# Kernel optimization log

Hardware: AMD Instinct MI355X
Metric: run time of the kernel (lower is better)

Reference implementation:

```python
import jax, jax.numpy as jnp
import numpy as np

INV_SMOOTHNESS = 0.1  # matches __init__ default


def setup_inputs() -> dict:
    key = jax.random.key(0)
    B, N, W, H = 128, 64, 64, 64
    # polygon vertices in pixel coordinates [0, W) x [0, H)
    vertices = jax.random.uniform(key, (B, N, 2), dtype=jnp.float32) * jnp.array([W, H], jnp.float32)
    return {"vertices": vertices, "width": W, "height": H}


def reference(vertices, width, height):
    """Soft polygon rasterization (mode='mask').

    For every pixel p: d2 = min over edges of squared point-to-segment distance;
    sign = +1 if p inside polygon (even-odd rule) else -1;
    out = sigmoid(sign * d2 / inv_smoothness).
    Matches the native CUDA forward_rasterize for MODE_MASK.
    """
    B, N, _ = vertices.shape
    dt = vertices.dtype
    xs = jnp.arange(width, dtype=dt)
    ys = jnp.arange(height, dtype=dt)
    px, py = jnp.meshgrid(xs, ys, indexing="xy")         # [H, W]
    p = jnp.stack([px.ravel(), py.ravel()], axis=-1)       # [P, 2], P = H*W

    a = vertices                                           # [B, N, 2] edge start
    b = jnp.roll(vertices, -1, axis=1)                     # [B, N, 2] edge end
    d = b - a                                              # [B, N, 2]
    dd = jnp.maximum(jnp.sum(d * d, axis=-1), 1e-12)       # [B, N]

    # point-to-segment squared distance, vectorized over pixels and edges
    pa = p[None, :, None, :] - a[:, None, :, :]            # [B, P, N, 2]
    t = jnp.clip(jnp.einsum("bpnc,bnc->bpn", pa, d) / dd[:, None, :], 0.0, 1.0)
    diff = pa - t[..., None] * d[:, None, :, :]            # [B, P, N, 2]
    dist2 = jnp.sum(diff * diff, axis=-1)                  # [B, P, N]
    min_d2 = jnp.min(dist2, axis=-1)                       # [B, P]

    # even-odd (pnpoly) inside test
    x = p[:, 0][None, :, None]                             # [1, P, 1]
    y = p[:, 1][None, :, None]
    ax, ay = a[:, None, :, 0], a[:, None, :, 1]            # [B, 1, N]
    bx, by = b[:, None, :, 0], b[:, None, :, 1]
    cond = (ay > y) != (by > y)                            # edge straddles scanline
    denom = jnp.where(cond, by - ay, 1.0)
    x_int = (bx - ax) * (y - ay) / denom + ax              # edge x at scanline y
    crossings = jnp.sum((cond & (x < x_int)).astype(jnp.int32), axis=-1)  # [B, P]
    sign = jnp.where((crossings % 2) == 1, 1.0, -1.0).astype(dt)

    out = jax.nn.sigmoid(sign * min_d2 / INV_SMOOTHNESS)
    return out.reshape(B, height, width)
```

## Files before the change

kernel.cpp:

```cpp
#include <hip/hip_runtime.h>


#define EDGE(E0, E1, DA, DB)                                       \
    {                                                              \
        float pay  = py - E0.y;                                    \
        float pdyr = pay * E1.y;                                   \
        float xint = fmaf(pay, E1.z, E0.x);                        \
        bool  cond = (E0.y > py) != (E1.w > py);                   \
        float paxa = px0 - E0.x;                                   \
        float paxb = paxa + 1.0f;                                  \
        float ta = fminf(fmaxf(fmaf(paxa, E1.x, pdyr), 0.0f), 1.0f); \
        float tb = fminf(fmaxf(fmaf(paxb, E1.x, pdyr), 0.0f), 1.0f); \
        float exa = fmaf(-ta, E0.z, paxa);                         \
        float eya = fmaf(-ta, E0.w, pay);                          \
        float exb = fmaf(-tb, E0.z, paxb);                         \
        float eyb = fmaf(-tb, E0.w, pay);                          \
        DA = fmaf(exa, exa, eya * eya);                            \
        DB = fmaf(exb, exb, eyb * eyb);                            \
        pm0 ^= __ballot(cond && (px0 < xint));                     \
        pm1 ^= __ballot(cond && (px1 < xint));                     \
    }

__global__ __launch_bounds__(256, 4) void softpoly_kernel(
    const float* __restrict__ verts, float* __restrict__ out)
{
    __shared__ float4 e0[64];
    __shared__ float4 e1[64];

    const int tid = threadIdx.x;
    const int b   = blockIdx.x >> 3;

    if (tid < 64) {
        const float2* vp = (const float2*)(verts + (b << 7));
        float2 a = vp[tid];
        float2 c = vp[(tid + 1) & 63];
        float dx = c.x - a.x, dy = c.y - a.y;
        float dd = fmaxf(fmaf(dx, dx, dy * dy), 1e-12f);
        float rdd = 1.0f / dd;
        e0[tid] = make_float4(a.x, a.y, dx, dy);
        e1[tid] = make_float4(dx * rdd, dy * rdd, dx / dy, c.y);
    }
    __syncthreads();

    const int row = ((blockIdx.x & 7) << 3) + (tid >> 5);
    const float py  = (float)row;
    const float px0 = (float)((tid & 31) << 1);
    const float px1 = px0 + 1.0f;

    float md0 = 1e30f, md1 = 1e30f;
    unsigned long long pm0 = 0ull, pm1 = 0ull;

    #pragma unroll 2
    for (int n = 0; n < 64; n += 2) {
        const float4 A0 = e0[n],     A1 = e1[n];
        const float4 B0 = e0[n + 1], B1 = e1[n + 1];
        float dA0, dA1, dB0, dB1;
        EDGE(A0, A1, dA0, dA1)
        EDGE(B0, B1, dB0, dB1)
        md0 = fminf(md0, fminf(dA0, dB0));
        md1 = fminf(md1, fminf(dA1, dB1));
    }

    const int lane = tid & 63;
    const float s0 = ((pm0 >> lane) & 1ull) ? 10.0f : -10.0f;
    const float s1 = ((pm1 >> lane) & 1ull) ? 10.0f : -10.0f;
    float2 r;
    r.x = 1.0f / (1.0f + __expf(-s0 * md0));
    r.y = 1.0f / (1.0f + __expf(-s1 * md1));
    ((float2*)out)[(((b << 6) + row) << 5) + (tid & 31)] = r;
}

extern "C" void kernel_launch(void* const* d_in, const int* in_sizes, int n_in,
                              void* d_out, int out_size, void* d_ws, size_t ws_size,
                              hipStream_t stream) {
    const float* verts = (const float*)d_in[0];
    float* out = (float*)d_out;
    const int B = out_size >> 12;
    softpoly_kernel<<<dim3(B * 8), dim3(256), 0, stream>>>(verts, out);
}
```

Baseline: 16.06 us.

## Use packed FP32 math and four pixels per thread in soft polygon kernel

Each thread now covers four adjacent pixels instead of two, and the grid shrinks to four blocks per batch. The per-edge distance math uses inline-asm v_pk_fma/v_pk_mul/v_pk_add to handle two pixels per instruction. The aim is to amortize edge loads and per-edge scalar setup over more pixels and to halve the VALU instruction count for the distance computation. The trade-offs are higher register pressure, the removal of the occupancy hint from launch_bounds, and fewer blocks in flight.

After: 19.04 us. +18.5%, slower.

```diff
diff --git a/kernel.cpp b/kernel.cpp
--- a/kernel.cpp
+++ b/kernel.cpp
@@ -1,34 +1,57 @@
 #include <hip/hip_runtime.h>
 
 
-#define EDGE(E0, E1, DA, DB)                                       \
-    {                                                              \
-        float pay  = py - E0.y;                                    \
-        float pdyr = pay * E1.y;                                   \
-        float xint = fmaf(pay, E1.z, E0.x);                        \
-        bool  cond = (E0.y > py) != (E1.w > py);                   \
-        float paxa = px0 - E0.x;                                   \
-        float paxb = paxa + 1.0f;                                  \
-        float ta = fminf(fmaxf(fmaf(paxa, E1.x, pdyr), 0.0f), 1.0f); \
-        float tb = fminf(fmaxf(fmaf(paxb, E1.x, pdyr), 0.0f), 1.0f); \
-        float exa = fmaf(-ta, E0.z, paxa);                         \
-        float eya = fmaf(-ta, E0.w, pay);                          \
-        float exb = fmaf(-tb, E0.z, paxb);                         \
-        float eyb = fmaf(-tb, E0.w, pay);                          \
-        DA = fmaf(exa, exa, eya * eya);                            \
-        DB = fmaf(exb, exb, eyb * eyb);                            \
-        pm0 ^= __ballot(cond && (px0 < xint));                     \
-        pm1 ^= __ballot(cond && (px1 < xint));                     \
+typedef float f32x2 __attribute__((ext_vector_type(2)));
+typedef float f32x4 __attribute__((ext_vector_type(4)));
+
+#define PK_FMA(d,a,b,c)      asm("v_pk_fma_f32 %0, %1, %2, %3" : "=v"(d) : "v"(a), "v"(b), "v"(c))
+#define PK_MUL(d,a,b)        asm("v_pk_mul_f32 %0, %1, %2" : "=v"(d) : "v"(a), "v"(b))
+#define PK_FMA_BLO(d,a,B,c)  asm("v_pk_fma_f32 %0, %1, %2, %3 op_sel_hi:[1,0,1]" : "=v"(d) : "v"(a), "v"(B), "v"(c))
+#define PK_NFMA_BLO(d,a,B,c) asm("v_pk_fma_f32 %0, %1, %2, %3 op_sel_hi:[1,0,1] neg_lo:[1,0,0] neg_hi:[1,0,0]" : "=v"(d) : "v"(a), "v"(B), "v"(c))
+#define PK_NFMA_BHI(d,a,B,c) asm("v_pk_fma_f32 %0, %1, %2, %3 op_sel:[0,1,0] op_sel_hi:[1,1,1] neg_lo:[1,0,0] neg_hi:[1,0,0]" : "=v"(d) : "v"(a), "v"(B), "v"(c))
+#define PK_SUB_BLO(d,a,B)    asm("v_pk_add_f32 %0, %1, %2 op_sel_hi:[1,0] neg_lo:[0,1] neg_hi:[0,1]" : "=v"(d) : "v"(a), "v"(B))
+#define PK_SUB_BHI(d,a,B)    asm("v_pk_add_f32 %0, %1, %2 op_sel:[0,1] op_sel_hi:[1,1] neg_lo:[0,1] neg_hi:[0,1]" : "=v"(d) : "v"(a), "v"(B))
+#define PK_MUL_BHI(d,a,B)    asm("v_pk_mul_f32 %0, %1, %2 op_sel:[0,1] op_sel_hi:[1,1]" : "=v"(d) : "v"(a), "v"(B))
+
+#define EDGE(E0, E1, DA, DB)                                        \
+    {                                                               \
+        f32x2 E0lo = E0.xy, E0hi = E0.zw, E1lo = E1.xy;             \
+        f32x2 payv, pdyrv;                                          \
+        PK_SUB_BHI(payv, pyv, E0lo);           \
+        PK_MUL_BHI(pdyrv, payv, E1lo);         \
+        float xint = fmaf(payv.x, E1.z, E0.x);                      \
+        bool  cond = (E0.y > py) != (E1.w > py);                    \
+        f32x2 paxA, paxB, tA, tB, exA, exB, eyA, eyB, qA, qB;       \
+        PK_SUB_BLO(paxA, pxA, E0lo);           \
+        PK_SUB_BLO(paxB, pxB, E0lo);                                \
+        PK_FMA_BLO(tA, paxA, E1lo, pdyrv);     \
+        PK_FMA_BLO(tB, paxB, E1lo, pdyrv);                          \
+        tA.x = fminf(fmaxf(tA.x, 0.0f), 1.0f);          \
+        tA.y = fminf(fmaxf(tA.y, 0.0f), 1.0f);                      \
+        tB.x = fminf(fmaxf(tB.x, 0.0f), 1.0f);                      \
+        tB.y = fminf(fmaxf(tB.y, 0.0f), 1.0f);                      \
+        PK_NFMA_BLO(exA, tA, E0hi, paxA);      \
+        PK_NFMA_BLO(exB, tB, E0hi, paxB);                           \
+        PK_NFMA_BHI(eyA, tA, E0hi, payv);      \
+        PK_NFMA_BHI(eyB, tB, E0hi, payv);                           \
+        PK_MUL(qA, eyA, eyA);                                       \
+        PK_MUL(qB, eyB, eyB);                                       \
+        PK_FMA(DA, exA, exA, qA);              \
+        PK_FMA(DB, exB, exB, qB);                                   \
+        pm0 ^= __ballot(cond && (px0f < xint));                     \
+        pm1 ^= __ballot(cond && (px1f < xint));                     \
+        pm2 ^= __ballot(cond && (px2f < xint));                     \
+        pm3 ^= __ballot(cond && (px3f < xint));                     \
     }
 
-__global__ __launch_bounds__(256, 4) void softpoly_kernel(
+__global__ __launch_bounds__(256) void softpoly_kernel(
     const float* __restrict__ verts, float* __restrict__ out)
 {
-    __shared__ float4 e0[64];
-    __shared__ float4 e1[64];
+    __shared__ f32x4 e0[64];
+    __shared__ f32x4 e1[64];
 
     const int tid = threadIdx.x;
-    const int b   = blockIdx.x >> 3;
+    const int b   = blockIdx.x >> 2;
 
     if (tid < 64) {
         const float2* vp = (const float2*)(verts + (b << 7));
@@ -37,37 +60,45 @@
         float dx = c.x - a.x, dy = c.y - a.y;
         float dd = fmaxf(fmaf(dx, dx, dy * dy), 1e-12f);
         float rdd = 1.0f / dd;
-        e0[tid] = make_float4(a.x, a.y, dx, dy);
-        e1[tid] = make_float4(dx * rdd, dy * rdd, dx / dy, c.y);
+        e0[tid] = (f32x4){a.x, a.y, dx, dy};
+        e1[tid] = (f32x4){dx * rdd, dy * rdd, dx / dy, c.y};
     }
     __syncthreads();
 
-    const int row = ((blockIdx.x & 7) << 3) + (tid >> 5);
-    const float py  = (float)row;
-    const float px0 = (float)((tid & 31) << 1);
-    const float px1 = px0 + 1.0f;
+    const int row = ((blockIdx.x & 3) << 4) + (tid >> 4);
+    const float py   = (float)row;
+    const float px0f = (float)((tid & 15) << 2);
+    const float px1f = px0f + 1.0f, px2f = px0f + 2.0f, px3f = px0f + 3.0f;
+    const f32x2 pyv = {py, py};
+    const f32x2 pxA = {px0f, px1f}, pxB = {px2f, px3f};
 
-    float md0 = 1e30f, md1 = 1e30f;
-    unsigned long long pm0 = 0ull, pm1 = 0ull;
+    float md0 = 1e30f, md1 = 1e30f, md2 = 1e30f, md3 = 1e30f;
+    unsigned long long pm0 = 0ull, pm1 = 0ull, pm2 = 0ull, pm3 = 0ull;
 
     #pragma unroll 2
     for (int n = 0; n < 64; n += 2) {
-        const float4 A0 = e0[n],     A1 = e1[n];
-        const float4 B0 = e0[n + 1], B1 = e1[n + 1];
-        float dA0, dA1, dB0, dB1;
-        EDGE(A0, A1, dA0, dA1)
-        EDGE(B0, B1, dB0, dB1)
-        md0 = fminf(md0, fminf(dA0, dB0));
-        md1 = fminf(md1, fminf(dA1, dB1));
+        const f32x4 A0 = e0[n],     A1 = e1[n];
+        const f32x4 B0 = e0[n + 1], B1 = e1[n + 1];
+        f32x2 dAA, dAB, dBA, dBB;
+        EDGE(A0, A1, dAA, dAB)
+        EDGE(B0, B1, dBA, dBB)
+        md0 = fminf(md0, fminf(dAA.x, dBA.x));
+        md1 = fminf(md1, fminf(dAA.y, dBA.y));
+        md2 = fminf(md2, fminf(dAB.x, dBB.x));
+        md3 = fminf(md3, fminf(dAB.y, dBB.y));
     }
 
     const int lane = tid & 63;
     const float s0 = ((pm0 >> lane) & 1ull) ? 10.0f : -10.0f;
     const float s1 = ((pm1 >> lane) & 1ull) ? 10.0f : -10.0f;
-    float2 r;
+    const float s2 = ((pm2 >> lane) & 1ull) ? 10.0f : -10.0f;
+    const float s3 = ((pm3 >> lane) & 1ull) ? 10.0f : -10.0f;
+    float4 r;
     r.x = 1.0f / (1.0f + __expf(-s0 * md0));
     r.y = 1.0f / (1.0f + __expf(-s1 * md1));
-    ((float2*)out)[(((b << 6) + row) << 5) + (tid & 31)] = r;
+    r.z = 1.0f / (1.0f + __expf(-s2 * md2));
+    r.w = 1.0f / (1.0f + __expf(-s3 * md3));
+    ((float4*)out)[(b << 10) + (row << 4) + (tid & 15)] = r;
 }
 
 extern "C" void kernel_launch(void* const* d_in, const int* in_sizes, int n_in,
@@ -76,5 +107,5 @@
     const float* verts = (const float*)d_in[0];
     float* out = (float*)d_out;
     const int B = out_size >> 12;
-    softpoly_kernel<<<dim3(B * 8), dim3(256), 0, stream>>>(verts, out);
+    softpoly_kernel<<<dim3(B * 4), dim3(256), 0, stream>>>(verts, out);
 }
```

## Compute four pixels per thread and hoist crossing mask into shared ballots

Applied to the files above, without the earlier changes.

Each thread now handles four horizontally adjacent pixels instead of two, halving the grid to four blocks per polygon and amortizing per-edge scalar setup (pay, pdyr, crossing condition) over more pixels. The straddle test is computed once per edge as an XOR of two ballots and ANDed with per-pixel ballots, the x-intersection comparison is rewritten relative to the edge start, and clamping uses med3. Output is written as float4. The trade-off is higher register pressure (launch bounds lowered) and fewer blocks for latency hiding.

Result: faster. 15.21 us (-5.3%).

```diff
diff --git a/kernel.cpp b/kernel.cpp
--- a/kernel.cpp
+++ b/kernel.cpp
@@ -1,34 +1,16 @@
 #include <hip/hip_runtime.h>
 
 
-#define EDGE(E0, E1, DA, DB)                                       \
-    {                                                              \
-        float pay  = py - E0.y;                                    \
-        float pdyr = pay * E1.y;                                   \
-        float xint = fmaf(pay, E1.z, E0.x);                        \
-        bool  cond = (E0.y > py) != (E1.w > py);                   \
-        float paxa = px0 - E0.x;                                   \
-        float paxb = paxa + 1.0f;                                  \
-        float ta = fminf(fmaxf(fmaf(paxa, E1.x, pdyr), 0.0f), 1.0f); \
-        float tb = fminf(fmaxf(fmaf(paxb, E1.x, pdyr), 0.0f), 1.0f); \
-        float exa = fmaf(-ta, E0.z, paxa);                         \
-        float eya = fmaf(-ta, E0.w, pay);                          \
-        float exb = fmaf(-tb, E0.z, paxb);                         \
-        float eyb = fmaf(-tb, E0.w, pay);                          \
-        DA = fmaf(exa, exa, eya * eya);                            \
-        DB = fmaf(exb, exb, eyb * eyb);                            \
-        pm0 ^= __ballot(cond && (px0 < xint));                     \
-        pm1 ^= __ballot(cond && (px1 < xint));                     \
-    }
+typedef unsigned long long u64;
 
-__global__ __launch_bounds__(256, 4) void softpoly_kernel(
+__global__ __launch_bounds__(256, 2) void softpoly_kernel(
     const float* __restrict__ verts, float* __restrict__ out)
 {
     __shared__ float4 e0[64];
     __shared__ float4 e1[64];
 
     const int tid = threadIdx.x;
-    const int b   = blockIdx.x >> 3;
+    const int b   = blockIdx.x >> 2;
 
     if (tid < 64) {
         const float2* vp = (const float2*)(verts + (b << 7));
@@ -42,32 +24,83 @@
     }
     __syncthreads();
 
-    const int row = ((blockIdx.x & 7) << 3) + (tid >> 5);
+    const int row = ((blockIdx.x & 3) << 4) + (tid >> 4);
     const float py  = (float)row;
-    const float px0 = (float)((tid & 31) << 1);
-    const float px1 = px0 + 1.0f;
+    const float pxb = (float)((tid & 15) << 2);
 
-    float md0 = 1e30f, md1 = 1e30f;
-    unsigned long long pm0 = 0ull, pm1 = 0ull;
+    float md0 = 1e30f, md1 = 1e30f, md2 = 1e30f, md3 = 1e30f;
+    u64 pm0 = 0ull, pm1 = 0ull, pm2 = 0ull, pm3 = 0ull;
 
-    #pragma unroll 2
+    #pragma unroll 4
     for (int n = 0; n < 64; n += 2) {
         const float4 A0 = e0[n],     A1 = e1[n];
         const float4 B0 = e0[n + 1], B1 = e1[n + 1];
-        float dA0, dA1, dB0, dB1;
-        EDGE(A0, A1, dA0, dA1)
-        EDGE(B0, B1, dB0, dB1)
+        float dA0, dA1, dA2, dA3, dB0, dB1, dB2, dB3;
+        {
+            float pay  = py - A0.y;
+            float pdyr = pay * A1.y;
+            float xma  = pay * A1.z;
+            u64 cm = __ballot(A0.y > py) ^ __ballot(A1.w > py);
+            float pax0 = pxb - A0.x, pax1 = pax0 + 1.0f,
+                  pax2 = pax0 + 2.0f, pax3 = pax0 + 3.0f;
+            float t0 = __builtin_amdgcn_fmed3f(fmaf(pax0, A1.x, pdyr), 0.f, 1.f);
+            float t1 = __builtin_amdgcn_fmed3f(fmaf(pax1, A1.x, pdyr), 0.f, 1.f);
+            float t2 = __builtin_amdgcn_fmed3f(fmaf(pax2, A1.x, pdyr), 0.f, 1.f);
+            float t3 = __builtin_amdgcn_fmed3f(fmaf(pax3, A1.x, pdyr), 0.f, 1.f);
+            float ex0 = fmaf(-t0, A0.z, pax0), ey0 = fmaf(-t0, A0.w, pay);
+            float ex1 = fmaf(-t1, A0.z, pax1), ey1 = fmaf(-t1, A0.w, pay);
+            float ex2 = fmaf(-t2, A0.z, pax2), ey2 = fmaf(-t2, A0.w, pay);
+            float ex3 = fmaf(-t3, A0.z, pax3), ey3 = fmaf(-t3, A0.w, pay);
+            dA0 = fmaf(ex0, ex0, ey0 * ey0);
+            dA1 = fmaf(ex1, ex1, ey1 * ey1);
+            dA2 = fmaf(ex2, ex2, ey2 * ey2);
+            dA3 = fmaf(ex3, ex3, ey3 * ey3);
+            pm0 ^= cm & __ballot(pax0 < xma);
+            pm1 ^= cm & __ballot(pax1 < xma);
+            pm2 ^= cm & __ballot(pax2 < xma);
+            pm3 ^= cm & __ballot(pax3 < xma);
+        }
+        {
+            float pay  = py - B0.y;
+            float pdyr = pay * B1.y;
+            float xma  = pay * B1.z;
+            u64 cm = __ballot(B0.y > py) ^ __ballot(B1.w > py);
+            float pax0 = pxb - B0.x, pax1 = pax0 + 1.0f,
+                  pax2 = pax0 + 2.0f, pax3 = pax0 + 3.0f;
+            float t0 = __builtin_amdgcn_fmed3f(fmaf(pax0, B1.x, pdyr), 0.f, 1.f);
+            float t1 = __builtin_amdgcn_fmed3f(fmaf(pax1, B1.x, pdyr), 0.f, 1.f);
+            float t2 = __builtin_amdgcn_fmed3f(fmaf(pax2, B1.x, pdyr), 0.f, 1.f);
+            float t3 = __builtin_amdgcn_fmed3f(fmaf(pax3, B1.x, pdyr), 0.f, 1.f);
+            float ex0 = fmaf(-t0, B0.z, pax0), ey0 = fmaf(-t0, B0.w, pay);
+            float ex1 = fmaf(-t1, B0.z, pax1), ey1 = fmaf(-t1, B0.w, pay);
+            float ex2 = fmaf(-t2, B0.z, pax2), ey2 = fmaf(-t2, B0.w, pay);
+            float ex3 = fmaf(-t3, B0.z, pax3), ey3 = fmaf(-t3, B0.w, pay);
+            dB0 = fmaf(ex0, ex0, ey0 * ey0);
+            dB1 = fmaf(ex1, ex1, ey1 * ey1);
+            dB2 = fmaf(ex2, ex2, ey2 * ey2);
+            dB3 = fmaf(ex3, ex3, ey3 * ey3);
+            pm0 ^= cm & __ballot(pax0 < xma);
+            pm1 ^= cm & __ballot(pax1 < xma);
+            pm2 ^= cm & __ballot(pax2 < xma);
+            pm3 ^= cm & __ballot(pax3 < xma);
+        }
         md0 = fminf(md0, fminf(dA0, dB0));
         md1 = fminf(md1, fminf(dA1, dB1));
+        md2 = fminf(md2, fminf(dA2, dB2));
+        md3 = fminf(md3, fminf(dA3, dB3));
     }
 
     const int lane = tid & 63;
     const float s0 = ((pm0 >> lane) & 1ull) ? 10.0f : -10.0f;
     const float s1 = ((pm1 >> lane) & 1ull) ? 10.0f : -10.0f;
-    float2 r;
+    const float s2 = ((pm2 >> lane) & 1ull) ? 10.0f : -10.0f;
+    const float s3 = ((pm3 >> lane) & 1ull) ? 10.0f : -10.0f;
+    float4 r;
     r.x = 1.0f / (1.0f + __expf(-s0 * md0));
     r.y = 1.0f / (1.0f + __expf(-s1 * md1));
-    ((float2*)out)[(((b << 6) + row) << 5) + (tid & 31)] = r;
+    r.z = 1.0f / (1.0f + __expf(-s2 * md2));
+    r.w = 1.0f / (1.0f + __expf(-s3 * md3));
+    ((float4*)out)[(b << 10) + (row << 4) + (tid & 15)] = r;
 }
 
 extern "C" void kernel_launch(void* const* d_in, const int* in_sizes, int n_in,
@@ -76,5 +109,5 @@
     const float* verts = (const float*)d_in[0];
     float* out = (float*)d_out;
     const int B = out_size >> 12;
-    softpoly_kernel<<<dim3(B * 8), dim3(256), 0, stream>>>(verts, out);
+    softpoly_kernel<<<dim3(B * 4), dim3(256), 0, stream>>>(verts, out);
 }
```
